# Optimization experiments

Hardware: AMD Instinct MI355X
Metric: run time of the kernel (lower is better)

## Reference

```python
import jax, jax.numpy as jnp
import numpy as np

B, S, D = 4, 4096, 256

def setup_inputs() -> dict:
    key = jax.random.key(0)
    ks = jax.random.split(key, 9)
    sc = 1.0 / np.sqrt(D)
    return {
        "v": jax.random.normal(ks[0], (B, S, D), jnp.float32),
        "k": jax.random.normal(ks[1], (B, S, D), jnp.float32),
        "q": jax.random.normal(ks[2], (B, S, D), jnp.float32),
        "Wq": jax.random.normal(ks[3], (D, D), jnp.float32) * sc,
        "bq": jnp.zeros((D,), jnp.float32),
        "Wk": jax.random.normal(ks[4], (D, D), jnp.float32) * sc,
        "bk": jnp.zeros((D,), jnp.float32),
        "Wv": jax.random.normal(ks[5], (D, D), jnp.float32) * sc,
        "bv": jnp.zeros((D,), jnp.float32),
    }

def reference(v, k, q, Wq, bq, Wk, bk, Wv, bv):
    d_model = q.shape[-1]
    seq_len = q.shape[-2]
    qp = q @ Wq + bq                      # [B,S,D]
    kp = k @ Wk + bk
    vp = v @ Wv + bv
    # scores [B,S,S], scaled then MULTIPLIED by lower-triangular mask (faithful to original)
    scores = jnp.einsum('bqd,bkd->bqk', qp, kp) / jnp.sqrt(jnp.float32(d_model))
    mask = jnp.tril(jnp.ones((seq_len, seq_len), scores.dtype))
    scores = scores * mask
    attn = jax.nn.softmax(scores, axis=-1)
    return qp + jnp.einsum('bqk,bkd->bqd', attn, vp)
```

## Files before the change

kernel.cpp:

```cpp
#include <hip/hip_runtime.h>
#include <hip/hip_bf16.h>


typedef __bf16 bf16x8 __attribute__((ext_vector_type(8)));
typedef float f32x4 __attribute__((ext_vector_type(4)));
typedef float f32x16 __attribute__((ext_vector_type(16)));
typedef unsigned int u32x4 __attribute__((ext_vector_type(4)));

#define MASKV -3.0e38f

__device__ __forceinline__ unsigned short f2bf_u(float f) {
  unsigned u = __float_as_uint(f);
  u += 0x7fffu + ((u >> 16) & 1u);
  return (unsigned short)(u >> 16);
}
__device__ __forceinline__ float bf2f(unsigned u16) {
  return __uint_as_float(u16 << 16);
}
__device__ __forceinline__ unsigned short cvt_bf(float f) {
  return __builtin_bit_cast(unsigned short, (__bf16)f);
}

__global__ __launch_bounds__(256) void wt_kernel(
    const float* __restrict__ Wq, const float* __restrict__ Wk, const float* __restrict__ Wv,
    unsigned short* __restrict__ WTq, unsigned short* __restrict__ WTk, unsigned short* __restrict__ WTv) {
  int j = blockIdx.x & 255;
  int wsel = blockIdx.x >> 8;
  const float* W = wsel == 0 ? Wq : (wsel == 1 ? Wk : Wv);
  unsigned short* WT = wsel == 0 ? WTq : (wsel == 1 ? WTk : WTv);
  int k = threadIdx.x;
  WT[j * 256 + k] = f2bf_u(W[k * 256 + j]);
}

__global__ __launch_bounds__(256) void proj_all_kernel(
    const float* __restrict__ q_in, const float* __restrict__ k_in, const float* __restrict__ v_in,
    const unsigned short* __restrict__ WTq, const unsigned short* __restrict__ WTk,
    const unsigned short* __restrict__ WTv,
    const float* __restrict__ bq, const float* __restrict__ bk, const float* __restrict__ bv,
    unsigned short* __restrict__ qpb, unsigned short* __restrict__ kpb,
    float* __restrict__ vpf, unsigned short* __restrict__ vptb) {
  int mode = blockIdx.y;
  const float* X = mode == 0 ? q_in : (mode == 1 ? k_in : v_in);
  const unsigned short* WT = mode == 0 ? WTq : (mode == 1 ? WTk : WTv);
  const float* bias = mode == 0 ? bq : (mode == 1 ? bk : bv);

  int rt = blockIdx.x;
  int tid = threadIdx.x;
  int w = tid >> 6, l = tid & 63, g = l >> 4, lm = l & 15;
  int arow = rt * 64 + w * 16 + lm;

  f32x4 acc[16];
#pragma unroll
  for (int i = 0; i < 16; i++) acc[i] = (f32x4){0.f, 0.f, 0.f, 0.f};

#pragma unroll
  for (int kb = 0; kb < 256; kb += 32) {
    const float* ap = X + arow * 256 + kb + 8 * g;
    float4 a0 = *(const float4*)ap;
    float4 a1 = *(const float4*)(ap + 4);
    bf16x8 af;
    af[0] = (__bf16)a0.x; af[1] = (__bf16)a0.y; af[2] = (__bf16)a0.z; af[3] = (__bf16)a0.w;
    af[4] = (__bf16)a1.x; af[5] = (__bf16)a1.y; af[6] = (__bf16)a1.z; af[7] = (__bf16)a1.w;
#pragma unroll
    for (int nt = 0; nt < 16; nt++) {
      bf16x8 bf = *(const bf16x8*)(WT + (nt * 16 + lm) * 256 + kb + 8 * g);
      acc[nt] = __builtin_amdgcn_mfma_f32_16x16x32_bf16(af, bf, acc[nt], 0, 0, 0);
    }
  }

#pragma unroll
  for (int nt = 0; nt < 16; nt++) {
    int col = nt * 16 + lm;
    float bb = bias[col];
#pragma unroll
    for (int r = 0; r < 4; r++) {
      int orow = rt * 64 + w * 16 + 4 * g + r;
      float v = acc[nt][r] + bb;
      int idx = orow * 256 + col;
      if (mode == 0) {
        qpb[idx] = f2bf_u(v * 0.0625f);
      } else if (mode == 1) {
        kpb[idx] = f2bf_u(v * 1.4426950408889634f);
      } else {
        vpf[idx] = v;
        int b = orow >> 12, sidx = orow & 4095;
        vptb[(((size_t)b * 128 + (sidx >> 5)) * 256 + col) * 32 + (sidx & 31)] = f2bf_u(v);
      }
    }
  }
}

__global__ __launch_bounds__(256) void scan1(const float* __restrict__ vpf, float* __restrict__ ctot) {
  int c = blockIdx.x, b = blockIdx.y, d = threadIdx.x;
  const float* base = vpf + (b * 4096 + c * 64) * 256 + d;
  float acc = 0.f;
#pragma unroll 4
  for (int r = 0; r < 64; r++) acc += base[r * 256];
  ctot[(b * 64 + c) * 256 + d] = acc;
}

__global__ __launch_bounds__(256) void scan2(const float* __restrict__ vpf, const float* __restrict__ ctot,
                                             unsigned short* __restrict__ suffv) {
  int c = blockIdx.x, b = blockIdx.y, d = threadIdx.x;
  float acc = 0.f;
  for (int c2 = c + 1; c2 < 64; c2++) acc += ctot[(b * 64 + c2) * 256 + d];
  const float* base = vpf + (b * 4096 + c * 64) * 256 + d;
  unsigned short* sbase = suffv + (b * 4096 + c * 64) * 256 + d;
  for (int r = 63; r >= 0; r--) {
    sbase[r * 256] = f2bf_u(acc);
    acc += base[r * 256];
  }
}

__global__ __launch_bounds__(256, 2) void attn8_kernel(
    const unsigned short* __restrict__ qpb, const unsigned short* __restrict__ kpb,
    const unsigned short* __restrict__ vptb,
    unsigned short* __restrict__ slot01,
    unsigned short* __restrict__ slot23,
    unsigned short* __restrict__ slot45,
    float* __restrict__ mz) {
  extern __shared__ char smem[];

  int bid = blockIdx.x;
  int low = bid & 7;
  int b = low >> 1, shi = low & 1;
  int j = bid >> 3;
  int jd3 = j / 3;
  int qb = 31 - jd3;
  int s = shi * 3 + (j - jd3 * 3);
  int NT = 4 * (qb + 1);
  int t0 = (s * NT) / 6, t1 = ((s + 1) * NT) / 6;

  int tid = threadIdx.x;
  int wv = tid >> 6, l = tid & 63;
  int hi = l >> 5, r32 = l & 31;
  int vsw = (r32 >> 1) & 3;
  int ksw = r32 & 7;

  int qwave = qb * 128 + 32 * wv;
  int qglob = qwave + r32;

  bf16x8 qf[16];
  const unsigned short* qsrc = qpb + (size_t)(b * 4096 + qwave + r32) * 256;
#pragma unroll
  for (int st = 0; st < 16; st++) qf[st] = *(const bf16x8*)(qsrc + st * 16 + 8 * hi);

  f32x16 zero16;
#pragma unroll
  for (int ee = 0; ee < 16; ee++) zero16[ee] = 0.f;
  f32x16 O[8];
#pragma unroll
  for (int dt = 0; dt < 8; dt++) O[dt] = zero16;
  float m_ = -1e30f, Z_ = 0.f;

  const unsigned short* kbase0 = kpb + (size_t)b * 4096 * 256;
  const unsigned short* vbase0 = vptb + (size_t)b * 128 * 256 * 32;

  auto STAGE = [&](int bi, int kt) {
    char* Kdst = smem + bi * 16384;
    char* Vdst = smem + 32768 + bi * 16384;
    const unsigned short* ksrc = kbase0 + (size_t)kt * 32 * 256;
    const unsigned short* vtile = vbase0 + (size_t)kt * 256 * 32;
#pragma unroll
    for (int j2 = 0; j2 < 4; j2++) {
      int ch = wv * 4 + j2;
      int row = ch * 2 + (l >> 5);
      int cc = (l & 31) ^ (row & 7);
      __builtin_amdgcn_global_load_lds(
          (const __attribute__((address_space(1))) unsigned int*)(ksrc + row * 256 + cc * 8),
          (__attribute__((address_space(3))) unsigned int*)(Kdst + ch * 1024), 16, 0, 0);
    }
#pragma unroll
    for (int j2 = 0; j2 < 4; j2++) {
      int ch = wv * 4 + j2;
      int d = ch * 16 + (l >> 2);
      int cc = (l & 3) ^ ((l >> 3) & 3);
      __builtin_amdgcn_global_load_lds(
          (const __attribute__((address_space(1))) unsigned int*)(vtile + d * 32 + cc * 8),
          (__attribute__((address_space(3))) unsigned int*)(Vdst + ch * 1024), 16, 0, 0);
    }
  };

  if (t0 < t1) {
    STAGE(0, t0);
    if (t0 + 1 < t1) STAGE(1, t0 + 1);
  }

  for (int kt = t0; kt < t1; kt++) {
    int cur = (kt - t0) & 1;
    int kb2 = kt * 32;

    if (kt + 1 < t1) asm volatile("s_waitcnt vmcnt(8)" ::: "memory");
    else             asm volatile("s_waitcnt vmcnt(0)" ::: "memory");
    __builtin_amdgcn_s_barrier();
    __builtin_amdgcn_sched_barrier(0);

    if (kb2 <= qwave + 31) {
      const char* Kp = smem + cur * 16384;
      const char* Vp = smem + 32768 + cur * 16384;

      f32x16 St;
      __builtin_amdgcn_s_setprio(1);
      {
        bf16x8 kf = *(const bf16x8*)(Kp + r32 * 512 + ((hi ^ ksw) * 16));
        St = __builtin_amdgcn_mfma_f32_32x32x16_bf16(kf, qf[0], zero16, 0, 0, 0);
      }
#pragma unroll
      for (int st = 1; st < 16; st++) {
        bf16x8 kf = *(const bf16x8*)(Kp + r32 * 512 + (((2 * st + hi) ^ ksw) * 16));
        St = __builtin_amdgcn_mfma_f32_32x32x16_bf16(kf, qf[st], St, 0, 0, 0);
      }
      __builtin_amdgcn_s_setprio(0);

      if (kb2 + 31 > qwave) {
#pragma unroll
        for (int r = 0; r < 16; r++) {
          int kg = kb2 + (r & 3) + 8 * (r >> 2) + 4 * hi;
          if (kg > qglob) St[r] = MASKV;
        }
      }

      float mx = fmaxf(fmaxf(fmaxf(St[0], St[1]), fmaxf(St[2], St[3])),
                       fmaxf(fmaxf(St[4], St[5]), fmaxf(St[6], St[7])));
      float mx2 = fmaxf(fmaxf(fmaxf(St[8], St[9]), fmaxf(St[10], St[11])),
                        fmaxf(fmaxf(St[12], St[13]), fmaxf(St[14], St[15])));
      mx = fmaxf(mx, mx2);
      mx = fmaxf(mx, __shfl_xor(mx, 32));
      bool upd = __any(mx > m_ + 8.f);
      if (upd) {
        float mn = fmaxf(m_, mx);
        float scl = exp2f(m_ - mn);
        m_ = mn;
        Z_ *= scl;
#pragma unroll
        for (int r = 0; r < 16; r++) {
          int qr = (r & 3) + 8 * (r >> 2) + 4 * hi;
          float sb = __uint_as_float(
              (unsigned)__builtin_amdgcn_ds_bpermute(qr * 4, (int)__float_as_uint(scl)));
#pragma unroll
          for (int dt = 0; dt < 8; dt++) O[dt][r] *= sb;
        }
      }
      float p[16];
#pragma unroll
      for (int r = 0; r < 16; r++) p[r] = exp2f(St[r] - m_);
      float rs = ((p[0] + p[1]) + (p[2] + p[3])) + ((p[4] + p[5]) + (p[6] + p[7])) +
                 (((p[8] + p[9]) + (p[10] + p[11])) + ((p[12] + p[13]) + (p[14] + p[15])));
      rs += __shfl_xor(rs, 32);
      Z_ += rs;

      unsigned X[8];
#pragma unroll
      for (int i = 0; i < 8; i++)
        X[i] = (unsigned)cvt_bf(p[2 * i]) | ((unsigned)cvt_bf(p[2 * i + 1]) << 16);
      unsigned Y0 = (unsigned)__shfl_xor((int)X[0], 32);
      unsigned Y1 = (unsigned)__shfl_xor((int)X[1], 32);
      unsigned Y2 = (unsigned)__shfl_xor((int)X[2], 32);
      unsigned Y3 = (unsigned)__shfl_xor((int)X[3], 32);
      unsigned Y4 = (unsigned)__shfl_xor((int)X[4], 32);
      unsigned Y5 = (unsigned)__shfl_xor((int)X[5], 32);
      unsigned Y6 = (unsigned)__shfl_xor((int)X[6], 32);
      unsigned Y7 = (unsigned)__shfl_xor((int)X[7], 32);
      u32x4 A0, A1;
      A0[0] = hi ? Y2 : X[0]; A0[1] = hi ? Y3 : X[1];
      A0[2] = hi ? X[2] : Y0; A0[3] = hi ? X[3] : Y1;
      A1[0] = hi ? Y6 : X[4]; A1[1] = hi ? Y7 : X[5];
      A1[2] = hi ? X[6] : Y4; A1[3] = hi ? X[7] : Y5;
      bf16x8 pa0 = __builtin_bit_cast(bf16x8, A0);
      bf16x8 pa1 = __builtin_bit_cast(bf16x8, A1);

      __builtin_amdgcn_s_setprio(1);
#pragma unroll
      for (int dt = 0; dt < 8; dt++) {
        bf16x8 vf0 = *(const bf16x8*)(Vp + (dt * 32 + r32) * 64 + ((hi ^ vsw) * 16));
        O[dt] = __builtin_amdgcn_mfma_f32_32x32x16_bf16(pa0, vf0, O[dt], 0, 0, 0);
      }
#pragma unroll
      for (int dt = 0; dt < 8; dt++) {
        bf16x8 vf1 = *(const bf16x8*)(Vp + (dt * 32 + r32) * 64 + (((2 + hi) ^ vsw) * 16));
        O[dt] = __builtin_amdgcn_mfma_f32_32x32x16_bf16(pa1, vf1, O[dt], 0, 0, 0);
      }
      __builtin_amdgcn_s_setprio(0);
    }

    __builtin_amdgcn_sched_barrier(0);
    __builtin_amdgcn_s_barrier();
    if (kt + 2 < t1) STAGE(cur, kt + 2);
  }

  int grow_base = b * 4096 + qwave;
  if (hi == 0) {
    float* mzm = mz + s * 32768;
    mzm[grow_base + r32] = m_;
    mzm[16384 + grow_base + r32] = Z_;
  }
#pragma unroll
  for (int r = 0; r < 16; r++) {
    int qr = (r & 3) + 8 * (r >> 2) + 4 * hi;
    size_t grow = (size_t)(grow_base + qr);
#pragma unroll
    for (int dt = 0; dt < 8; dt++) {
      int dcol = dt * 32 + r32;
      unsigned short vb = cvt_bf(O[dt][r]);
      if (s < 2)
        slot01[grow * 512 + (size_t)s * 256 + dcol] = vb;
      else if (s < 4)
        slot23[(size_t)(s - 2) * 4194304 + grow * 256 + dcol] = vb;
      else
        slot45[(size_t)(s - 4) * 4194304 + grow * 256 + dcol] = vb;
    }
  }
}

__global__ __launch_bounds__(256) void combine6_kernel(
    const float* __restrict__ mz,
    const unsigned short* __restrict__ slot23, const unsigned short* __restrict__ slot45,
    const unsigned short* __restrict__ qpb, const unsigned short* __restrict__ suffv,
    float* __restrict__ out) {
  int grow = blockIdx.x * 4 + (threadIdx.x >> 6);
  int col = (threadIdx.x & 63) * 4;
  const unsigned short* slot01 = (const unsigned short*)out;

  float mv[6], Zv[6];
#pragma unroll
  for (int s = 0; s < 6; s++) {
    const float* mzm = mz + s * 32768;
    mv[s] = mzm[grow];
    Zv[s] = mzm[16384 + grow];
  }
  float M = mv[0];
#pragma unroll
  for (int s = 1; s < 6; s++) M = fmaxf(M, mv[s]);
  float fs[6], Zm = 0.f;
#pragma unroll
  for (int s = 0; s < 6; s++) {
    fs[s] = exp2f(mv[s] - M);
    Zm += Zv[s] * fs[s];
  }

  int q = grow & 4095;
  int nmask = 4095 - q;
  float scl, e0, Zf;
  if (nmask > 0) {
    float Mf = fmaxf(M, 0.f);
    scl = exp2f(M - Mf);
    e0 = exp2f(-Mf);
    Zf = Zm * scl + (float)nmask * e0;
  } else {
    scl = 1.f; e0 = 0.f; Zf = Zm;
  }
  float rZ = 1.f / Zf;
  float a[6];
#pragma unroll
  for (int s = 0; s < 6; s++) a[s] = fs[s] * scl * rZ;
  float asv = e0 * rZ;

  size_t base = (size_t)grow * 256 + col;
  uint2 ss[6];
  ss[0] = *(const uint2*)(slot01 + (size_t)grow * 512 + col);
  ss[1] = *(const uint2*)(slot01 + (size_t)grow * 512 + 256 + col);
  ss[2] = *(const uint2*)(slot23 + base);
  ss[3] = *(const uint2*)(slot23 + 4194304 + base);
  ss[4] = *(const uint2*)(slot45 + base);
  ss[5] = *(const uint2*)(slot45 + 4194304 + base);
  uint2 qpr = *(const uint2*)(qpb + base);
  uint2 svu = *(const uint2*)(suffv + base);

  __syncthreads();

  float4 res;
  res.x = 16.f * bf2f(qpr.x & 0xffff) + bf2f(svu.x & 0xffff) * asv;
  res.y = 16.f * bf2f(qpr.x >> 16) + bf2f(svu.x >> 16) * asv;
  res.z = 16.f * bf2f(qpr.y & 0xffff) + bf2f(svu.y & 0xffff) * asv;
  res.w = 16.f * bf2f(qpr.y >> 16) + bf2f(svu.y >> 16) * asv;
#pragma unroll
  for (int s = 0; s < 6; s++) {
    res.x += bf2f(ss[s].x & 0xffff) * a[s];
    res.y += bf2f(ss[s].x >> 16) * a[s];
    res.z += bf2f(ss[s].y & 0xffff) * a[s];
    res.w += bf2f(ss[s].y >> 16) * a[s];
  }
  *(float4*)&out[base] = res;
}

extern "C" void kernel_launch(void* const* d_in, const int* in_sizes, int n_in,
                              void* d_out, int out_size, void* d_ws, size_t ws_size,
                              hipStream_t stream) {
  const float* v_in = (const float*)d_in[0];
  const float* k_in = (const float*)d_in[1];
  const float* q_in = (const float*)d_in[2];
  const float* Wq = (const float*)d_in[3];
  const float* bq = (const float*)d_in[4];
  const float* Wk = (const float*)d_in[5];
  const float* bk = (const float*)d_in[6];
  const float* Wv = (const float*)d_in[7];
  const float* bv = (const float*)d_in[8];
  float* out = (float*)d_out;

  char* p = (char*)d_ws;
  unsigned short* slot45 = (unsigned short*)(p + 0);
  float* vpf = (float*)(p + 16777216);
  unsigned short* slot23 = (unsigned short*)(p + 16777216);
  unsigned short* suffv = (unsigned short*)(p + 33554432);
  unsigned short* qpb = (unsigned short*)(p + 41943040);
  unsigned short* kpb = (unsigned short*)(p + 50331648);
  unsigned short* vptb = (unsigned short*)(p + 58720256);
  float* mz = (float*)(p + 67108864);
  unsigned short* WTq = (unsigned short*)(p + 67895296);
  unsigned short* WTk = (unsigned short*)(p + 68026368);
  unsigned short* WTv = (unsigned short*)(p + 68157440);
  float* ctot = (float*)(p + 68288512);
  unsigned short* slot01 = (unsigned short*)d_out;

  hipFuncSetAttribute((const void*)attn8_kernel,
                      hipFuncAttributeMaxDynamicSharedMemorySize, 65536);

  wt_kernel<<<768, 256, 0, stream>>>(Wq, Wk, Wv, WTq, WTk, WTv);
  proj_all_kernel<<<dim3(256, 3), 256, 0, stream>>>(q_in, k_in, v_in, WTq, WTk, WTv,
                                                    bq, bk, bv, qpb, kpb, vpf, vptb);
  scan1<<<dim3(64, 4), 256, 0, stream>>>(vpf, ctot);
  scan2<<<dim3(64, 4), 256, 0, stream>>>(vpf, ctot, suffv);
  attn8_kernel<<<768, 256, 65536, stream>>>(qpb, kpb, vptb, slot01, slot23, slot45, mz);
  combine6_kernel<<<4096, 256, 0, stream>>>(mz, slot23, slot45, qpb, suffv, out);
}
```

Baseline: 184.7 us.

## Enlarge attention tiles to 256 queries × 64 keys and split head dim across blocks

Rebuilds the attention kernel around 512-thread blocks, each covering 256 query rows against 64-key tiles, while splitting the 256-wide value dimension into two halves handled by separate blocks. The V transpose layout moves to 64-key chunks and the LDS swizzles are updated to match. The goal is more K/V reuse per staged tile and fewer barriers per key. In exchange the QK^T work is done twice (once per value half), LDS use grows to 96KB, and register pressure at 512 threads may limit occupancy.

Result: slower. 189.3 us (+2.5%).

```diff
diff --git a/kernel.cpp b/kernel.cpp
--- a/kernel.cpp
+++ b/kernel.cpp
@@ -84,7 +84,7 @@
       } else {
         vpf[idx] = v;
         int b = orow >> 12, sidx = orow & 4095;
-        vptb[(((size_t)b * 128 + (sidx >> 5)) * 256 + col) * 32 + (sidx & 31)] = f2bf_u(v);
+        vptb[(((size_t)b * 64 + (sidx >> 6)) * 256 + col) * 64 + (sidx & 63)] = f2bf_u(v);
       }
     }
   }
@@ -112,7 +112,7 @@
   }
 }
 
-__global__ __launch_bounds__(256, 2) void attn8_kernel(
+__global__ __launch_bounds__(512, 2) void attn9_kernel(
     const unsigned short* __restrict__ qpb, const unsigned short* __restrict__ kpb,
     const unsigned short* __restrict__ vptb,
     unsigned short* __restrict__ slot01,
@@ -125,19 +125,20 @@
   int low = bid & 7;
   int b = low >> 1, shi = low & 1;
   int j = bid >> 3;
-  int jd3 = j / 3;
-  int qb = 31 - jd3;
-  int s = shi * 3 + (j - jd3 * 3);
-  int NT = 4 * (qb + 1);
+  int dh = j & 1;
+  int v = j >> 1;
+  int vd3 = v / 3;
+  int qt = 15 - vd3;
+  int s = shi * 3 + (v - vd3 * 3);
+  int NT = 4 * (qt + 1);
   int t0 = (s * NT) / 6, t1 = ((s + 1) * NT) / 6;
 
   int tid = threadIdx.x;
   int wv = tid >> 6, l = tid & 63;
   int hi = l >> 5, r32 = l & 31;
-  int vsw = (r32 >> 1) & 3;
-  int ksw = r32 & 7;
-
-  int qwave = qb * 128 + 32 * wv;
+  int vsw = r32 & 7;
+
+  int qwave = qt * 256 + 32 * wv;
   int qglob = qwave + r32;
 
   bf16x8 qf[16];
@@ -148,36 +149,34 @@
   f32x16 zero16;
 #pragma unroll
   for (int ee = 0; ee < 16; ee++) zero16[ee] = 0.f;
-  f32x16 O[8];
-#pragma unroll
-  for (int dt = 0; dt < 8; dt++) O[dt] = zero16;
+  f32x16 O[4];
+#pragma unroll
+  for (int dt = 0; dt < 4; dt++) O[dt] = zero16;
   float m_ = -1e30f, Z_ = 0.f;
 
   const unsigned short* kbase0 = kpb + (size_t)b * 4096 * 256;
-  const unsigned short* vbase0 = vptb + (size_t)b * 128 * 256 * 32;
+  const unsigned short* vbase0 = vptb + (size_t)b * 64 * 256 * 64 + (size_t)dh * 128 * 64;
 
   auto STAGE = [&](int bi, int kt) {
-    char* Kdst = smem + bi * 16384;
-    char* Vdst = smem + 32768 + bi * 16384;
-    const unsigned short* ksrc = kbase0 + (size_t)kt * 32 * 256;
-    const unsigned short* vtile = vbase0 + (size_t)kt * 256 * 32;
-#pragma unroll
-    for (int j2 = 0; j2 < 4; j2++) {
-      int ch = wv * 4 + j2;
-      int row = ch * 2 + (l >> 5);
-      int cc = (l & 31) ^ (row & 7);
+    char* Kdst = smem + bi * 32768;
+    char* Vdst = smem + 65536 + bi * 16384;
+    const unsigned short* ksrc = kbase0 + (size_t)kt * 64 * 256;
+    const unsigned short* vtile = vbase0 + (size_t)kt * 256 * 64;
+#pragma unroll
+    for (int i = 0; i < 4; i++) {
+      int ch = i * 512 + tid;
+      int row = ch >> 5, cc = ch & 31;
       __builtin_amdgcn_global_load_lds(
-          (const __attribute__((address_space(1))) unsigned int*)(ksrc + row * 256 + cc * 8),
-          (__attribute__((address_space(3))) unsigned int*)(Kdst + ch * 1024), 16, 0, 0);
-    }
-#pragma unroll
-    for (int j2 = 0; j2 < 4; j2++) {
-      int ch = wv * 4 + j2;
-      int d = ch * 16 + (l >> 2);
-      int cc = (l & 3) ^ ((l >> 3) & 3);
+          (const __attribute__((address_space(1))) unsigned int*)(ksrc + row * 256 + ((cc ^ (row & 31)) * 8)),
+          (__attribute__((address_space(3))) unsigned int*)(Kdst + ch * 16), 16, 0, 0);
+    }
+#pragma unroll
+    for (int i = 0; i < 2; i++) {
+      int ch = i * 512 + tid;
+      int dl = ch >> 3, cs = ch & 7;
       __builtin_amdgcn_global_load_lds(
-          (const __attribute__((address_space(1))) unsigned int*)(vtile + d * 32 + cc * 8),
-          (__attribute__((address_space(3))) unsigned int*)(Vdst + ch * 1024), 16, 0, 0);
+          (const __attribute__((address_space(1))) unsigned int*)(vtile + dl * 64 + ((cs ^ (dl & 7)) * 8)),
+          (__attribute__((address_space(3))) unsigned int*)(Vdst + ch * 16), 16, 0, 0);
     }
   };
 
@@ -188,43 +187,47 @@
 
   for (int kt = t0; kt < t1; kt++) {
     int cur = (kt - t0) & 1;
-    int kb2 = kt * 32;
-
-    if (kt + 1 < t1) asm volatile("s_waitcnt vmcnt(8)" ::: "memory");
+    int kb2 = kt * 64;
+
+    if (kt + 1 < t1) asm volatile("s_waitcnt vmcnt(6)" ::: "memory");
     else             asm volatile("s_waitcnt vmcnt(0)" ::: "memory");
     __builtin_amdgcn_s_barrier();
     __builtin_amdgcn_sched_barrier(0);
 
     if (kb2 <= qwave + 31) {
-      const char* Kp = smem + cur * 16384;
-      const char* Vp = smem + 32768 + cur * 16384;
-
-      f32x16 St;
+      const char* Kp = smem + cur * 32768;
+      const char* Vp = smem + 65536 + cur * 16384;
+
+      f32x16 St0, St1;
       __builtin_amdgcn_s_setprio(1);
       {
-        bf16x8 kf = *(const bf16x8*)(Kp + r32 * 512 + ((hi ^ ksw) * 16));
-        St = __builtin_amdgcn_mfma_f32_32x32x16_bf16(kf, qf[0], zero16, 0, 0, 0);
+        bf16x8 kf0 = *(const bf16x8*)(Kp + r32 * 512 + ((hi ^ r32) & 31) * 16);
+        bf16x8 kf1 = *(const bf16x8*)(Kp + (32 + r32) * 512 + ((hi ^ r32) & 31) * 16);
+        St0 = __builtin_amdgcn_mfma_f32_32x32x16_bf16(kf0, qf[0], zero16, 0, 0, 0);
+        St1 = __builtin_amdgcn_mfma_f32_32x32x16_bf16(kf1, qf[0], zero16, 0, 0, 0);
       }
 #pragma unroll
       for (int st = 1; st < 16; st++) {
-        bf16x8 kf = *(const bf16x8*)(Kp + r32 * 512 + (((2 * st + hi) ^ ksw) * 16));
-        St = __builtin_amdgcn_mfma_f32_32x32x16_bf16(kf, qf[st], St, 0, 0, 0);
+        int cc = ((2 * st + hi) ^ r32) & 31;
+        bf16x8 kf0 = *(const bf16x8*)(Kp + r32 * 512 + cc * 16);
+        bf16x8 kf1 = *(const bf16x8*)(Kp + (32 + r32) * 512 + cc * 16);
+        St0 = __builtin_amdgcn_mfma_f32_32x32x16_bf16(kf0, qf[st], St0, 0, 0, 0);
+        St1 = __builtin_amdgcn_mfma_f32_32x32x16_bf16(kf1, qf[st], St1, 0, 0, 0);
       }
       __builtin_amdgcn_s_setprio(0);
 
-      if (kb2 + 31 > qwave) {
+      if (kb2 + 63 > qwave) {
 #pragma unroll
         for (int r = 0; r < 16; r++) {
           int kg = kb2 + (r & 3) + 8 * (r >> 2) + 4 * hi;
-          if (kg > qglob) St[r] = MASKV;
+          if (kg > qglob) St0[r] = MASKV;
+          if (kg + 32 > qglob) St1[r] = MASKV;
         }
       }
 
-      float mx = fmaxf(fmaxf(fmaxf(St[0], St[1]), fmaxf(St[2], St[3])),
-                       fmaxf(fmaxf(St[4], St[5]), fmaxf(St[6], St[7])));
-      float mx2 = fmaxf(fmaxf(fmaxf(St[8], St[9]), fmaxf(St[10], St[11])),
-                        fmaxf(fmaxf(St[12], St[13]), fmaxf(St[14], St[15])));
-      mx = fmaxf(mx, mx2);
+      float mx = fmaxf(St0[0], St1[0]);
+#pragma unroll
+      for (int r = 1; r < 16; r++) mx = fmaxf(mx, fmaxf(St0[r], St1[r]));
       mx = fmaxf(mx, __shfl_xor(mx, 32));
       bool upd = __any(mx > m_ + 8.f);
       if (upd) {
@@ -238,49 +241,89 @@
           float sb = __uint_as_float(
               (unsigned)__builtin_amdgcn_ds_bpermute(qr * 4, (int)__float_as_uint(scl)));
 #pragma unroll
-          for (int dt = 0; dt < 8; dt++) O[dt][r] *= sb;
+          for (int dt = 0; dt < 4; dt++) O[dt][r] *= sb;
         }
       }
-      float p[16];
-#pragma unroll
-      for (int r = 0; r < 16; r++) p[r] = exp2f(St[r] - m_);
-      float rs = ((p[0] + p[1]) + (p[2] + p[3])) + ((p[4] + p[5]) + (p[6] + p[7])) +
-                 (((p[8] + p[9]) + (p[10] + p[11])) + ((p[12] + p[13]) + (p[14] + p[15])));
+      float rs = 0.f;
+#pragma unroll
+      for (int r = 0; r < 16; r++) {
+        St0[r] = exp2f(St0[r] - m_);
+        St1[r] = exp2f(St1[r] - m_);
+        rs += St0[r] + St1[r];
+      }
       rs += __shfl_xor(rs, 32);
       Z_ += rs;
 
-      unsigned X[8];
-#pragma unroll
-      for (int i = 0; i < 8; i++)
-        X[i] = (unsigned)cvt_bf(p[2 * i]) | ((unsigned)cvt_bf(p[2 * i + 1]) << 16);
-      unsigned Y0 = (unsigned)__shfl_xor((int)X[0], 32);
-      unsigned Y1 = (unsigned)__shfl_xor((int)X[1], 32);
-      unsigned Y2 = (unsigned)__shfl_xor((int)X[2], 32);
-      unsigned Y3 = (unsigned)__shfl_xor((int)X[3], 32);
-      unsigned Y4 = (unsigned)__shfl_xor((int)X[4], 32);
-      unsigned Y5 = (unsigned)__shfl_xor((int)X[5], 32);
-      unsigned Y6 = (unsigned)__shfl_xor((int)X[6], 32);
-      unsigned Y7 = (unsigned)__shfl_xor((int)X[7], 32);
-      u32x4 A0, A1;
-      A0[0] = hi ? Y2 : X[0]; A0[1] = hi ? Y3 : X[1];
-      A0[2] = hi ? X[2] : Y0; A0[3] = hi ? X[3] : Y1;
-      A1[0] = hi ? Y6 : X[4]; A1[1] = hi ? Y7 : X[5];
-      A1[2] = hi ? X[6] : Y4; A1[3] = hi ? X[7] : Y5;
-      bf16x8 pa0 = __builtin_bit_cast(bf16x8, A0);
-      bf16x8 pa1 = __builtin_bit_cast(bf16x8, A1);
-
-      __builtin_amdgcn_s_setprio(1);
-#pragma unroll
-      for (int dt = 0; dt < 8; dt++) {
-        bf16x8 vf0 = *(const bf16x8*)(Vp + (dt * 32 + r32) * 64 + ((hi ^ vsw) * 16));
-        O[dt] = __builtin_amdgcn_mfma_f32_32x32x16_bf16(pa0, vf0, O[dt], 0, 0, 0);
-      }
-#pragma unroll
-      for (int dt = 0; dt < 8; dt++) {
-        bf16x8 vf1 = *(const bf16x8*)(Vp + (dt * 32 + r32) * 64 + (((2 + hi) ^ vsw) * 16));
-        O[dt] = __builtin_amdgcn_mfma_f32_32x32x16_bf16(pa1, vf1, O[dt], 0, 0, 0);
-      }
-      __builtin_amdgcn_s_setprio(0);
+      {
+        unsigned X0 = (unsigned)cvt_bf(St0[0]) | ((unsigned)cvt_bf(St0[1]) << 16);
+        unsigned X1 = (unsigned)cvt_bf(St0[2]) | ((unsigned)cvt_bf(St0[3]) << 16);
+        unsigned X2 = (unsigned)cvt_bf(St0[4]) | ((unsigned)cvt_bf(St0[5]) << 16);
+        unsigned X3 = (unsigned)cvt_bf(St0[6]) | ((unsigned)cvt_bf(St0[7]) << 16);
+        unsigned X4 = (unsigned)cvt_bf(St0[8]) | ((unsigned)cvt_bf(St0[9]) << 16);
+        unsigned X5 = (unsigned)cvt_bf(St0[10]) | ((unsigned)cvt_bf(St0[11]) << 16);
+        unsigned X6 = (unsigned)cvt_bf(St0[12]) | ((unsigned)cvt_bf(St0[13]) << 16);
+        unsigned X7 = (unsigned)cvt_bf(St0[14]) | ((unsigned)cvt_bf(St0[15]) << 16);
+        unsigned Y0 = (unsigned)__shfl_xor((int)X0, 32);
+        unsigned Y1 = (unsigned)__shfl_xor((int)X1, 32);
+        unsigned Y2 = (unsigned)__shfl_xor((int)X2, 32);
+        unsigned Y3 = (unsigned)__shfl_xor((int)X3, 32);
+        unsigned Y4 = (unsigned)__shfl_xor((int)X4, 32);
+        unsigned Y5 = (unsigned)__shfl_xor((int)X5, 32);
+        unsigned Y6 = (unsigned)__shfl_xor((int)X6, 32);
+        unsigned Y7 = (unsigned)__shfl_xor((int)X7, 32);
+        u32x4 A0, A1;
+        A0[0] = hi ? Y2 : X0; A0[1] = hi ? Y3 : X1;
+        A0[2] = hi ? X2 : Y0; A0[3] = hi ? X3 : Y1;
+        A1[0] = hi ? Y6 : X4; A1[1] = hi ? Y7 : X5;
+        A1[2] = hi ? X6 : Y4; A1[3] = hi ? X7 : Y5;
+        bf16x8 pa0 = __builtin_bit_cast(bf16x8, A0);
+        bf16x8 pa1 = __builtin_bit_cast(bf16x8, A1);
+        __builtin_amdgcn_s_setprio(1);
+#pragma unroll
+        for (int dt = 0; dt < 4; dt++) {
+          const char* vrow = Vp + (dt * 32 + r32) * 128;
+          bf16x8 vf0 = *(const bf16x8*)(vrow + ((hi ^ vsw) * 16));
+          O[dt] = __builtin_amdgcn_mfma_f32_32x32x16_bf16(pa0, vf0, O[dt], 0, 0, 0);
+          bf16x8 vf1 = *(const bf16x8*)(vrow + (((2 + hi) ^ vsw) * 16));
+          O[dt] = __builtin_amdgcn_mfma_f32_32x32x16_bf16(pa1, vf1, O[dt], 0, 0, 0);
+        }
+        __builtin_amdgcn_s_setprio(0);
+      }
+      {
+        unsigned X0 = (unsigned)cvt_bf(St1[0]) | ((unsigned)cvt_bf(St1[1]) << 16);
+        unsigned X1 = (unsigned)cvt_bf(St1[2]) | ((unsigned)cvt_bf(St1[3]) << 16);
+        unsigned X2 = (unsigned)cvt_bf(St1[4]) | ((unsigned)cvt_bf(St1[5]) << 16);
+        unsigned X3 = (unsigned)cvt_bf(St1[6]) | ((unsigned)cvt_bf(St1[7]) << 16);
+        unsigned X4 = (unsigned)cvt_bf(St1[8]) | ((unsigned)cvt_bf(St1[9]) << 16);
+        unsigned X5 = (unsigned)cvt_bf(St1[10]) | ((unsigned)cvt_bf(St1[11]) << 16);
+        unsigned X6 = (unsigned)cvt_bf(St1[12]) | ((unsigned)cvt_bf(St1[13]) << 16);
+        unsigned X7 = (unsigned)cvt_bf(St1[14]) | ((unsigned)cvt_bf(St1[15]) << 16);
+        unsigned Y0 = (unsigned)__shfl_xor((int)X0, 32);
+        unsigned Y1 = (unsigned)__shfl_xor((int)X1, 32);
+        unsigned Y2 = (unsigned)__shfl_xor((int)X2, 32);
+        unsigned Y3 = (unsigned)__shfl_xor((int)X3, 32);
+        unsigned Y4 = (unsigned)__shfl_xor((int)X4, 32);
+        unsigned Y5 = (unsigned)__shfl_xor((int)X5, 32);
+        unsigned Y6 = (unsigned)__shfl_xor((int)X6, 32);
+        unsigned Y7 = (unsigned)__shfl_xor((int)X7, 32);
+        u32x4 A2, A3;
+        A2[0] = hi ? Y2 : X0; A2[1] = hi ? Y3 : X1;
+        A2[2] = hi ? X2 : Y0; A2[3] = hi ? X3 : Y1;
+        A3[0] = hi ? Y6 : X4; A3[1] = hi ? Y7 : X5;
+        A3[2] = hi ? X6 : Y4; A3[3] = hi ? X7 : Y5;
+        bf16x8 pa2 = __builtin_bit_cast(bf16x8, A2);
+        bf16x8 pa3 = __builtin_bit_cast(bf16x8, A3);
+        __builtin_amdgcn_s_setprio(1);
+#pragma unroll
+        for (int dt = 0; dt < 4; dt++) {
+          const char* vrow = Vp + (dt * 32 + r32) * 128;
+          bf16x8 vf2 = *(const bf16x8*)(vrow + (((4 + hi) ^ vsw) * 16));
+          O[dt] = __builtin_amdgcn_mfma_f32_32x32x16_bf16(pa2, vf2, O[dt], 0, 0, 0);
+          bf16x8 vf3 = *(const bf16x8*)(vrow + (((6 + hi) ^ vsw) * 16));
+          O[dt] = __builtin_amdgcn_mfma_f32_32x32x16_bf16(pa3, vf3, O[dt], 0, 0, 0);
+        }
+        __builtin_amdgcn_s_setprio(0);
+      }
     }
 
     __builtin_amdgcn_sched_barrier(0);
@@ -289,7 +332,7 @@
   }
 
   int grow_base = b * 4096 + qwave;
-  if (hi == 0) {
+  if (dh == 0 && hi == 0) {
     float* mzm = mz + s * 32768;
     mzm[grow_base + r32] = m_;
     mzm[16384 + grow_base + r32] = Z_;
@@ -299,8 +342,8 @@
     int qr = (r & 3) + 8 * (r >> 2) + 4 * hi;
     size_t grow = (size_t)(grow_base + qr);
 #pragma unroll
-    for (int dt = 0; dt < 8; dt++) {
-      int dcol = dt * 32 + r32;
+    for (int dt = 0; dt < 4; dt++) {
+      int dcol = dh * 128 + dt * 32 + r32;
       unsigned short vb = cvt_bf(O[dt][r]);
       if (s < 2)
         slot01[grow * 512 + (size_t)s * 256 + dcol] = vb;
@@ -412,14 +455,14 @@
   float* ctot = (float*)(p + 68288512);
   unsigned short* slot01 = (unsigned short*)d_out;
 
-  hipFuncSetAttribute((const void*)attn8_kernel,
-                      hipFuncAttributeMaxDynamicSharedMemorySize, 65536);
+  hipFuncSetAttribute((const void*)attn9_kernel,
+                      hipFuncAttributeMaxDynamicSharedMemorySize, 98304);
 
   wt_kernel<<<768, 256, 0, stream>>>(Wq, Wk, Wv, WTq, WTk, WTv);
   proj_all_kernel<<<dim3(256, 3), 256, 0, stream>>>(q_in, k_in, v_in, WTq, WTk, WTv,
                                                     bq, bk, bv, qpb, kpb, vpf, vptb);
   scan1<<<dim3(64, 4), 256, 0, stream>>>(vpf, ctot);
   scan2<<<dim3(64, 4), 256, 0, stream>>>(vpf, ctot, suffv);
-  attn8_kernel<<<768, 256, 65536, stream>>>(qpb, kpb, vptb, slot01, slot23, slot45, mz);
+  attn9_kernel<<<768, 512, 98304, stream>>>(qpb, kpb, vptb, slot01, slot23, slot45, mz);
   combine6_kernel<<<4096, 256, 0, stream>>>(mz, slot23, slot45, qpb, suffv, out);
 }
```

## Replace double-buffered LDS DMA with register-staged single buffer and padded LDS

Applied to the files above, without the earlier changes.

The attention kernel drops its 64KB double-buffered LDS tiles filled by global_load_lds and uses a single padded static LDS buffer (about 37KB). The next K/V tile is prefetched into registers during compute and written to LDS after a barrier. Padding replaces the XOR swizzle for bank-conflict avoidance, and launch bounds rise to 3 blocks per CU to raise occupancy. In exchange it adds two barriers per tile, extra VGPR pressure from the register staging, and a store-to-LDS step that is no longer overlapped with compute.

Result: slower. 375.2 us (+103.1%).

```diff
diff --git a/kernel.cpp b/kernel.cpp
--- a/kernel.cpp
+++ b/kernel.cpp
@@ -112,14 +112,15 @@
   }
 }
 
-__global__ __launch_bounds__(256, 2) void attn8_kernel(
+__global__ __launch_bounds__(256, 3) void attn10_kernel(
     const unsigned short* __restrict__ qpb, const unsigned short* __restrict__ kpb,
     const unsigned short* __restrict__ vptb,
     unsigned short* __restrict__ slot01,
     unsigned short* __restrict__ slot23,
     unsigned short* __restrict__ slot45,
     float* __restrict__ mz) {
-  extern __shared__ char smem[];
+  __shared__ unsigned short Klds[32][264];
+  __shared__ unsigned short Vlds[256][40];
 
   int bid = blockIdx.x;
   int low = bid & 7;
@@ -134,8 +135,6 @@
   int tid = threadIdx.x;
   int wv = tid >> 6, l = tid & 63;
   int hi = l >> 5, r32 = l & 31;
-  int vsw = (r32 >> 1) & 3;
-  int ksw = r32 & 7;
 
   int qwave = qb * 128 + 32 * wv;
   int qglob = qwave + r32;
@@ -156,58 +155,59 @@
   const unsigned short* kbase0 = kpb + (size_t)b * 4096 * 256;
   const unsigned short* vbase0 = vptb + (size_t)b * 128 * 256 * 32;
 
-  auto STAGE = [&](int bi, int kt) {
-    char* Kdst = smem + bi * 16384;
-    char* Vdst = smem + 32768 + bi * 16384;
+  uint4 kreg[4], vreg[4];
+
+  auto LOADREG = [&](int kt) {
     const unsigned short* ksrc = kbase0 + (size_t)kt * 32 * 256;
     const unsigned short* vtile = vbase0 + (size_t)kt * 256 * 32;
 #pragma unroll
-    for (int j2 = 0; j2 < 4; j2++) {
-      int ch = wv * 4 + j2;
-      int row = ch * 2 + (l >> 5);
-      int cc = (l & 31) ^ (row & 7);
-      __builtin_amdgcn_global_load_lds(
-          (const __attribute__((address_space(1))) unsigned int*)(ksrc + row * 256 + cc * 8),
-          (__attribute__((address_space(3))) unsigned int*)(Kdst + ch * 1024), 16, 0, 0);
-    }
-#pragma unroll
-    for (int j2 = 0; j2 < 4; j2++) {
-      int ch = wv * 4 + j2;
-      int d = ch * 16 + (l >> 2);
-      int cc = (l & 3) ^ ((l >> 3) & 3);
-      __builtin_amdgcn_global_load_lds(
-          (const __attribute__((address_space(1))) unsigned int*)(vtile + d * 32 + cc * 8),
-          (__attribute__((address_space(3))) unsigned int*)(Vdst + ch * 1024), 16, 0, 0);
+    for (int i = 0; i < 4; i++) {
+      int ch = i * 256 + tid;
+      kreg[i] = *(const uint4*)(ksrc + (ch >> 5) * 256 + (ch & 31) * 8);
+    }
+#pragma unroll
+    for (int i = 0; i < 4; i++) {
+      int ch = i * 256 + tid;
+      vreg[i] = *(const uint4*)(vtile + (ch >> 2) * 32 + (ch & 3) * 8);
     }
   };
+  auto DSWRITE = [&]() {
+#pragma unroll
+    for (int i = 0; i < 4; i++) {
+      int ch = i * 256 + tid;
+      *(uint4*)((char*)Klds + (ch >> 5) * 528 + (ch & 31) * 16) = kreg[i];
+    }
+#pragma unroll
+    for (int i = 0; i < 4; i++) {
+      int ch = i * 256 + tid;
+      *(uint4*)((char*)Vlds + (ch >> 2) * 80 + (ch & 3) * 16) = vreg[i];
+    }
+  };
 
   if (t0 < t1) {
-    STAGE(0, t0);
-    if (t0 + 1 < t1) STAGE(1, t0 + 1);
-  }
-
-  for (int kt = t0; kt < t1; kt++) {
-    int cur = (kt - t0) & 1;
-    int kb2 = kt * 32;
-
-    if (kt + 1 < t1) asm volatile("s_waitcnt vmcnt(8)" ::: "memory");
-    else             asm volatile("s_waitcnt vmcnt(0)" ::: "memory");
+    LOADREG(t0);
+    asm volatile("s_waitcnt vmcnt(0)" ::: "memory");
+    DSWRITE();
+    asm volatile("s_waitcnt lgkmcnt(0)" ::: "memory");
     __builtin_amdgcn_s_barrier();
     __builtin_amdgcn_sched_barrier(0);
+  }
+
+  for (int kt = t0; kt < t1; kt++) {
+    int kb2 = kt * 32;
+    bool more = (kt + 1 < t1);
+    if (more) LOADREG(kt + 1);
 
     if (kb2 <= qwave + 31) {
-      const char* Kp = smem + cur * 16384;
-      const char* Vp = smem + 32768 + cur * 16384;
-
       f32x16 St;
       __builtin_amdgcn_s_setprio(1);
       {
-        bf16x8 kf = *(const bf16x8*)(Kp + r32 * 512 + ((hi ^ ksw) * 16));
+        bf16x8 kf = *(const bf16x8*)((const char*)Klds + r32 * 528 + hi * 16);
         St = __builtin_amdgcn_mfma_f32_32x32x16_bf16(kf, qf[0], zero16, 0, 0, 0);
       }
 #pragma unroll
       for (int st = 1; st < 16; st++) {
-        bf16x8 kf = *(const bf16x8*)(Kp + r32 * 512 + (((2 * st + hi) ^ ksw) * 16));
+        bf16x8 kf = *(const bf16x8*)((const char*)Klds + r32 * 528 + (2 * st + hi) * 16);
         St = __builtin_amdgcn_mfma_f32_32x32x16_bf16(kf, qf[st], St, 0, 0, 0);
       }
       __builtin_amdgcn_s_setprio(0);
@@ -272,20 +272,25 @@
       __builtin_amdgcn_s_setprio(1);
 #pragma unroll
       for (int dt = 0; dt < 8; dt++) {
-        bf16x8 vf0 = *(const bf16x8*)(Vp + (dt * 32 + r32) * 64 + ((hi ^ vsw) * 16));
+        const char* vrow = (const char*)Vlds + (dt * 32 + r32) * 80;
+        bf16x8 vf0 = *(const bf16x8*)(vrow + hi * 16);
         O[dt] = __builtin_amdgcn_mfma_f32_32x32x16_bf16(pa0, vf0, O[dt], 0, 0, 0);
-      }
-#pragma unroll
-      for (int dt = 0; dt < 8; dt++) {
-        bf16x8 vf1 = *(const bf16x8*)(Vp + (dt * 32 + r32) * 64 + (((2 + hi) ^ vsw) * 16));
+        bf16x8 vf1 = *(const bf16x8*)(vrow + (2 + hi) * 16);
         O[dt] = __builtin_amdgcn_mfma_f32_32x32x16_bf16(pa1, vf1, O[dt], 0, 0, 0);
       }
       __builtin_amdgcn_s_setprio(0);
     }
 
-    __builtin_amdgcn_sched_barrier(0);
-    __builtin_amdgcn_s_barrier();
-    if (kt + 2 < t1) STAGE(cur, kt + 2);
+    if (more) {
+      asm volatile("s_waitcnt lgkmcnt(0)" ::: "memory");
+      __builtin_amdgcn_s_barrier();
+      __builtin_amdgcn_sched_barrier(0);
+      asm volatile("s_waitcnt vmcnt(0)" ::: "memory");
+      DSWRITE();
+      asm volatile("s_waitcnt lgkmcnt(0)" ::: "memory");
+      __builtin_amdgcn_s_barrier();
+      __builtin_amdgcn_sched_barrier(0);
+    }
   }
 
   int grow_base = b * 4096 + qwave;
@@ -412,14 +417,11 @@
   float* ctot = (float*)(p + 68288512);
   unsigned short* slot01 = (unsigned short*)d_out;
 
-  hipFuncSetAttribute((const void*)attn8_kernel,
-                      hipFuncAttributeMaxDynamicSharedMemorySize, 65536);
-
   wt_kernel<<<768, 256, 0, stream>>>(Wq, Wk, Wv, WTq, WTk, WTv);
   proj_all_kernel<<<dim3(256, 3), 256, 0, stream>>>(q_in, k_in, v_in, WTq, WTk, WTv,
                                                     bq, bk, bv, qpb, kpb, vpf, vptb);
   scan1<<<dim3(64, 4), 256, 0, stream>>>(vpf, ctot);
   scan2<<<dim3(64, 4), 256, 0, stream>>>(vpf, ctot, suffv);
-  attn8_kernel<<<768, 256, 65536, stream>>>(qpb, kpb, vptb, slot01, slot23, slot45, mz);
+  attn10_kernel<<<768, 256, 0, stream>>>(qpb, kpb, vptb, slot01, slot23, slot45, mz);
   combine6_kernel<<<4096, 256, 0, stream>>>(mz, slot23, slot45, qpb, suffv, out);
 }
```

## Process key tiles in pairs per barrier and split suffix scan into finer chunks

Applied to the files above, without the earlier changes.

The attention loop now handles two staged K/V tiles per iteration and refills both buffers after the pair, instead of refilling one buffer per tile. The scan kernels use 16-row chunks over 256 chunks per batch instead of 64-row chunks, giving four times as many blocks. The pairing changes how load latency overlaps with compute: the second tile waits on vmcnt(0), so prefetch overlap may be reduced. The finer scan adds parallelism but makes scan2's prefix loop over chunk totals longer, and ctot now needs four times the space.

New measurement: 202.0 us. 1.09x slower.

```diff
diff --git a/kernel.cpp b/kernel.cpp
--- a/kernel.cpp
+++ b/kernel.cpp
@@ -92,27 +92,27 @@
 
 __global__ __launch_bounds__(256) void scan1(const float* __restrict__ vpf, float* __restrict__ ctot) {
   int c = blockIdx.x, b = blockIdx.y, d = threadIdx.x;
-  const float* base = vpf + (b * 4096 + c * 64) * 256 + d;
+  const float* base = vpf + (b * 4096 + c * 16) * 256 + d;
   float acc = 0.f;
-#pragma unroll 4
-  for (int r = 0; r < 64; r++) acc += base[r * 256];
-  ctot[(b * 64 + c) * 256 + d] = acc;
+#pragma unroll
+  for (int r = 0; r < 16; r++) acc += base[r * 256];
+  ctot[(b * 256 + c) * 256 + d] = acc;
 }
 
 __global__ __launch_bounds__(256) void scan2(const float* __restrict__ vpf, const float* __restrict__ ctot,
                                              unsigned short* __restrict__ suffv) {
   int c = blockIdx.x, b = blockIdx.y, d = threadIdx.x;
   float acc = 0.f;
-  for (int c2 = c + 1; c2 < 64; c2++) acc += ctot[(b * 64 + c2) * 256 + d];
-  const float* base = vpf + (b * 4096 + c * 64) * 256 + d;
-  unsigned short* sbase = suffv + (b * 4096 + c * 64) * 256 + d;
-  for (int r = 63; r >= 0; r--) {
+  for (int c2 = c + 1; c2 < 256; c2++) acc += ctot[(b * 256 + c2) * 256 + d];
+  const float* base = vpf + (b * 4096 + c * 16) * 256 + d;
+  unsigned short* sbase = suffv + (b * 4096 + c * 16) * 256 + d;
+  for (int r = 15; r >= 0; r--) {
     sbase[r * 256] = f2bf_u(acc);
     acc += base[r * 256];
   }
 }
 
-__global__ __launch_bounds__(256, 2) void attn8_kernel(
+__global__ __launch_bounds__(256, 2) void attn11_kernel(
     const unsigned short* __restrict__ qpb, const unsigned short* __restrict__ kpb,
     const unsigned short* __restrict__ vptb,
     unsigned short* __restrict__ slot01,
@@ -181,111 +181,121 @@
     }
   };
 
+  auto COMPUTE = [&](int bi, int kt) {
+    int kb2 = kt * 32;
+    if (kb2 > qwave + 31) return;
+    const char* Kp = smem + bi * 16384;
+    const char* Vp = smem + 32768 + bi * 16384;
+
+    f32x16 St;
+    __builtin_amdgcn_s_setprio(1);
+    {
+      bf16x8 kf = *(const bf16x8*)(Kp + r32 * 512 + ((hi ^ ksw) * 16));
+      St = __builtin_amdgcn_mfma_f32_32x32x16_bf16(kf, qf[0], zero16, 0, 0, 0);
+    }
+#pragma unroll
+    for (int st = 1; st < 16; st++) {
+      bf16x8 kf = *(const bf16x8*)(Kp + r32 * 512 + (((2 * st + hi) ^ ksw) * 16));
+      St = __builtin_amdgcn_mfma_f32_32x32x16_bf16(kf, qf[st], St, 0, 0, 0);
+    }
+    __builtin_amdgcn_s_setprio(0);
+
+    if (kb2 + 31 > qwave) {
+#pragma unroll
+      for (int r = 0; r < 16; r++) {
+        int kg = kb2 + (r & 3) + 8 * (r >> 2) + 4 * hi;
+        if (kg > qglob) St[r] = MASKV;
+      }
+    }
+
+    float mx = fmaxf(fmaxf(fmaxf(St[0], St[1]), fmaxf(St[2], St[3])),
+                     fmaxf(fmaxf(St[4], St[5]), fmaxf(St[6], St[7])));
+    float mx2 = fmaxf(fmaxf(fmaxf(St[8], St[9]), fmaxf(St[10], St[11])),
+                      fmaxf(fmaxf(St[12], St[13]), fmaxf(St[14], St[15])));
+    mx = fmaxf(mx, mx2);
+    mx = fmaxf(mx, __shfl_xor(mx, 32));
+    bool upd = __any(mx > m_ + 8.f);
+    if (upd) {
+      float mn = fmaxf(m_, mx);
+      float scl = exp2f(m_ - mn);
+      m_ = mn;
+      Z_ *= scl;
+#pragma unroll
+      for (int r = 0; r < 16; r++) {
+        int qr = (r & 3) + 8 * (r >> 2) + 4 * hi;
+        float sb = __uint_as_float(
+            (unsigned)__builtin_amdgcn_ds_bpermute(qr * 4, (int)__float_as_uint(scl)));
+#pragma unroll
+        for (int dt = 0; dt < 8; dt++) O[dt][r] *= sb;
+      }
+    }
+    float p[16];
+#pragma unroll
+    for (int r = 0; r < 16; r++) p[r] = exp2f(St[r] - m_);
+    float rs = ((p[0] + p[1]) + (p[2] + p[3])) + ((p[4] + p[5]) + (p[6] + p[7])) +
+               (((p[8] + p[9]) + (p[10] + p[11])) + ((p[12] + p[13]) + (p[14] + p[15])));
+    rs += __shfl_xor(rs, 32);
+    Z_ += rs;
+
+    unsigned X[8];
+#pragma unroll
+    for (int i = 0; i < 8; i++)
+      X[i] = (unsigned)cvt_bf(p[2 * i]) | ((unsigned)cvt_bf(p[2 * i + 1]) << 16);
+    unsigned Y0 = (unsigned)__shfl_xor((int)X[0], 32);
+    unsigned Y1 = (unsigned)__shfl_xor((int)X[1], 32);
+    unsigned Y2 = (unsigned)__shfl_xor((int)X[2], 32);
+    unsigned Y3 = (unsigned)__shfl_xor((int)X[3], 32);
+    unsigned Y4 = (unsigned)__shfl_xor((int)X[4], 32);
+    unsigned Y5 = (unsigned)__shfl_xor((int)X[5], 32);
+    unsigned Y6 = (unsigned)__shfl_xor((int)X[6], 32);
+    unsigned Y7 = (unsigned)__shfl_xor((int)X[7], 32);
+    u32x4 A0, A1;
+    A0[0] = hi ? Y2 : X[0]; A0[1] = hi ? Y3 : X[1];
+    A0[2] = hi ? X[2] : Y0; A0[3] = hi ? X[3] : Y1;
+    A1[0] = hi ? Y6 : X[4]; A1[1] = hi ? Y7 : X[5];
+    A1[2] = hi ? X[6] : Y4; A1[3] = hi ? X[7] : Y5;
+    bf16x8 pa0 = __builtin_bit_cast(bf16x8, A0);
+    bf16x8 pa1 = __builtin_bit_cast(bf16x8, A1);
+
+    __builtin_amdgcn_s_setprio(1);
+#pragma unroll
+    for (int dt = 0; dt < 8; dt++) {
+      bf16x8 vf0 = *(const bf16x8*)(Vp + (dt * 32 + r32) * 64 + ((hi ^ vsw) * 16));
+      O[dt] = __builtin_amdgcn_mfma_f32_32x32x16_bf16(pa0, vf0, O[dt], 0, 0, 0);
+    }
+#pragma unroll
+    for (int dt = 0; dt < 8; dt++) {
+      bf16x8 vf1 = *(const bf16x8*)(Vp + (dt * 32 + r32) * 64 + (((2 + hi) ^ vsw) * 16));
+      O[dt] = __builtin_amdgcn_mfma_f32_32x32x16_bf16(pa1, vf1, O[dt], 0, 0, 0);
+    }
+    __builtin_amdgcn_s_setprio(0);
+  };
+
   if (t0 < t1) {
     STAGE(0, t0);
     if (t0 + 1 < t1) STAGE(1, t0 + 1);
   }
 
-  for (int kt = t0; kt < t1; kt++) {
-    int cur = (kt - t0) & 1;
-    int kb2 = kt * 32;
-
-    if (kt + 1 < t1) asm volatile("s_waitcnt vmcnt(8)" ::: "memory");
-    else             asm volatile("s_waitcnt vmcnt(0)" ::: "memory");
+  for (int kt = t0; kt < t1; kt += 2) {
+    bool hasB = (kt + 1 < t1);
+
+    if (hasB) asm volatile("s_waitcnt vmcnt(8)" ::: "memory");
+    else      asm volatile("s_waitcnt vmcnt(0)" ::: "memory");
     __builtin_amdgcn_s_barrier();
     __builtin_amdgcn_sched_barrier(0);
-
-    if (kb2 <= qwave + 31) {
-      const char* Kp = smem + cur * 16384;
-      const char* Vp = smem + 32768 + cur * 16384;
-
-      f32x16 St;
-      __builtin_amdgcn_s_setprio(1);
-      {
-        bf16x8 kf = *(const bf16x8*)(Kp + r32 * 512 + ((hi ^ ksw) * 16));
-        St = __builtin_amdgcn_mfma_f32_32x32x16_bf16(kf, qf[0], zero16, 0, 0, 0);
-      }
-#pragma unroll
-      for (int st = 1; st < 16; st++) {
-        bf16x8 kf = *(const bf16x8*)(Kp + r32 * 512 + (((2 * st + hi) ^ ksw) * 16));
-        St = __builtin_amdgcn_mfma_f32_32x32x16_bf16(kf, qf[st], St, 0, 0, 0);
-      }
-      __builtin_amdgcn_s_setprio(0);
-
-      if (kb2 + 31 > qwave) {
-#pragma unroll
-        for (int r = 0; r < 16; r++) {
-          int kg = kb2 + (r & 3) + 8 * (r >> 2) + 4 * hi;
-          if (kg > qglob) St[r] = MASKV;
-        }
-      }
-
-      float mx = fmaxf(fmaxf(fmaxf(St[0], St[1]), fmaxf(St[2], St[3])),
-                       fmaxf(fmaxf(St[4], St[5]), fmaxf(St[6], St[7])));
-      float mx2 = fmaxf(fmaxf(fmaxf(St[8], St[9]), fmaxf(St[10], St[11])),
-                        fmaxf(fmaxf(St[12], St[13]), fmaxf(St[14], St[15])));
-      mx = fmaxf(mx, mx2);
-      mx = fmaxf(mx, __shfl_xor(mx, 32));
-      bool upd = __any(mx > m_ + 8.f);
-      if (upd) {
-        float mn = fmaxf(m_, mx);
-        float scl = exp2f(m_ - mn);
-        m_ = mn;
-        Z_ *= scl;
-#pragma unroll
-        for (int r = 0; r < 16; r++) {
-          int qr = (r & 3) + 8 * (r >> 2) + 4 * hi;
-          float sb = __uint_as_float(
-              (unsigned)__builtin_amdgcn_ds_bpermute(qr * 4, (int)__float_as_uint(scl)));
-#pragma unroll
-          for (int dt = 0; dt < 8; dt++) O[dt][r] *= sb;
-        }
-      }
-      float p[16];
-#pragma unroll
-      for (int r = 0; r < 16; r++) p[r] = exp2f(St[r] - m_);
-      float rs = ((p[0] + p[1]) + (p[2] + p[3])) + ((p[4] + p[5]) + (p[6] + p[7])) +
-                 (((p[8] + p[9]) + (p[10] + p[11])) + ((p[12] + p[13]) + (p[14] + p[15])));
-      rs += __shfl_xor(rs, 32);
-      Z_ += rs;
-
-      unsigned X[8];
-#pragma unroll
-      for (int i = 0; i < 8; i++)
-        X[i] = (unsigned)cvt_bf(p[2 * i]) | ((unsigned)cvt_bf(p[2 * i + 1]) << 16);
-      unsigned Y0 = (unsigned)__shfl_xor((int)X[0], 32);
-      unsigned Y1 = (unsigned)__shfl_xor((int)X[1], 32);
-      unsigned Y2 = (unsigned)__shfl_xor((int)X[2], 32);
-      unsigned Y3 = (unsigned)__shfl_xor((int)X[3], 32);
-      unsigned Y4 = (unsigned)__shfl_xor((int)X[4], 32);
-      unsigned Y5 = (unsigned)__shfl_xor((int)X[5], 32);
-      unsigned Y6 = (unsigned)__shfl_xor((int)X[6], 32);
-      unsigned Y7 = (unsigned)__shfl_xor((int)X[7], 32);
-      u32x4 A0, A1;
-      A0[0] = hi ? Y2 : X[0]; A0[1] = hi ? Y3 : X[1];
-      A0[2] = hi ? X[2] : Y0; A0[3] = hi ? X[3] : Y1;
-      A1[0] = hi ? Y6 : X[4]; A1[1] = hi ? Y7 : X[5];
-      A1[2] = hi ? X[6] : Y4; A1[3] = hi ? X[7] : Y5;
-      bf16x8 pa0 = __builtin_bit_cast(bf16x8, A0);
-      bf16x8 pa1 = __builtin_bit_cast(bf16x8, A1);
-
-      __builtin_amdgcn_s_setprio(1);
-#pragma unroll
-      for (int dt = 0; dt < 8; dt++) {
-        bf16x8 vf0 = *(const bf16x8*)(Vp + (dt * 32 + r32) * 64 + ((hi ^ vsw) * 16));
-        O[dt] = __builtin_amdgcn_mfma_f32_32x32x16_bf16(pa0, vf0, O[dt], 0, 0, 0);
-      }
-#pragma unroll
-      for (int dt = 0; dt < 8; dt++) {
-        bf16x8 vf1 = *(const bf16x8*)(Vp + (dt * 32 + r32) * 64 + (((2 + hi) ^ vsw) * 16));
-        O[dt] = __builtin_amdgcn_mfma_f32_32x32x16_bf16(pa1, vf1, O[dt], 0, 0, 0);
-      }
-      __builtin_amdgcn_s_setprio(0);
+    COMPUTE(0, kt);
+
+    if (hasB) {
+      asm volatile("s_waitcnt vmcnt(0)" ::: "memory");
+      __builtin_amdgcn_s_barrier();
+      __builtin_amdgcn_sched_barrier(0);
+      COMPUTE(1, kt + 1);
     }
 
     __builtin_amdgcn_sched_barrier(0);
     __builtin_amdgcn_s_barrier();
-    if (kt + 2 < t1) STAGE(cur, kt + 2);
+    if (kt + 2 < t1) STAGE(0, kt + 2);
+    if (kt + 3 < t1) STAGE(1, kt + 3);
   }
 
   int grow_base = b * 4096 + qwave;
@@ -412,14 +422,14 @@
   float* ctot = (float*)(p + 68288512);
   unsigned short* slot01 = (unsigned short*)d_out;
 
-  hipFuncSetAttribute((const void*)attn8_kernel,
+  hipFuncSetAttribute((const void*)attn11_kernel,
                       hipFuncAttributeMaxDynamicSharedMemorySize, 65536);
 
   wt_kernel<<<768, 256, 0, stream>>>(Wq, Wk, Wv, WTq, WTk, WTv);
   proj_all_kernel<<<dim3(256, 3), 256, 0, stream>>>(q_in, k_in, v_in, WTq, WTk, WTv,
                                                     bq, bk, bv, qpb, kpb, vpf, vptb);
-  scan1<<<dim3(64, 4), 256, 0, stream>>>(vpf, ctot);
-  scan2<<<dim3(64, 4), 256, 0, stream>>>(vpf, ctot, suffv);
-  attn8_kernel<<<768, 256, 65536, stream>>>(qpb, kpb, vptb, slot01, slot23, slot45, mz);
+  scan1<<<dim3(256, 4), 256, 0, stream>>>(vpf, ctot);
+  scan2<<<dim3(256, 4), 256, 0, stream>>>(vpf, ctot, suffv);
+  attn11_kernel<<<768, 256, 65536, stream>>>(qpb, kpb, vptb, slot01, slot23, slot45, mz);
   combine6_kernel<<<4096, 256, 0, stream>>>(mz, slot23, slot45, qpb, suffv, out);
 }
```
